# Kernel tuning notes

Measured on AMD Instinct MI355X. Metric: run time of the kernel, lower is better.

Reference implementation:

```python
import jax, jax.numpy as jnp
import numpy as np

# Multi-scale spatial shapes for a 704x256 input at strides 4/8/16/32
LEVEL_SHAPES = [(64, 176), (32, 88), (16, 44), (8, 22)]  # sum HW = 14960
NUM_CAMS, NUM_LEVELS, NUM_PTS, NUM_GROUPS = 6, 4, 13, 8
NUM_ANCHOR, EMBED_DIMS = 900, 256


def setup_inputs() -> dict:
    key = jax.random.key(0)
    ks = jax.random.split(key, 8)
    total_hw = sum(h * w for h, w in LEVEL_SHAPES)
    feat = jax.random.normal(ks[0], (1, NUM_CAMS, total_hw, EMBED_DIMS), jnp.float32)
    key_points = jax.random.uniform(ks[1], (1, NUM_ANCHOR, NUM_PTS, 3), jnp.float32)
    # near-identity projection so sampled locations spread over the image plane
    lidar2img = jnp.eye(4, dtype=jnp.float32)[None, None] + 0.05 * jax.random.normal(
        ks[2], (1, NUM_CAMS, 4, 4), jnp.float32)
    image_wh = jnp.ones((1, NUM_CAMS, 2), jnp.float32)
    instance_feature = jax.random.normal(ks[3], (1, NUM_ANCHOR, EMBED_DIMS), jnp.float32)
    anchor_embed = jax.random.normal(ks[4], (1, NUM_ANCHOR, EMBED_DIMS), jnp.float32)
    k_out = NUM_CAMS * NUM_LEVELS * NUM_PTS * NUM_GROUPS  # 2496
    weights_fc_w = jax.random.normal(ks[5], (k_out, EMBED_DIMS), jnp.float32) * 0.02
    weights_fc_b = jnp.zeros((k_out,), jnp.float32)
    out_proj_w = jax.random.normal(ks[6], (EMBED_DIMS, EMBED_DIMS), jnp.float32) * 0.02
    out_proj_b = jnp.zeros((EMBED_DIMS,), jnp.float32)
    return dict(feat=feat, key_points=key_points, lidar2img=lidar2img, image_wh=image_wh,
                instance_feature=instance_feature, anchor_embed=anchor_embed,
                weights_fc_w=weights_fc_w, weights_fc_b=weights_fc_b,
                out_proj_w=out_proj_w, out_proj_b=out_proj_b)


def _bilinear_sample(feat_flat, H, W, loc):
    # feat_flat: [bs, cams, H*W, C]; loc: [bs, cams, Q, 2] normalized to [0,1]
    x = loc[..., 0] * W - 0.5
    y = loc[..., 1] * H - 0.5
    x0 = jnp.floor(x); y0 = jnp.floor(y)
    wx1 = x - x0; wy1 = y - y0
    x0i = x0.astype(jnp.int32); y0i = y0.astype(jnp.int32)
    acc = jnp.zeros(loc.shape[:-1] + (feat_flat.shape[-1],), feat_flat.dtype)
    for dx, dy, w in ((0, 0, (1 - wx1) * (1 - wy1)), (1, 0, wx1 * (1 - wy1)),
                      (0, 1, (1 - wx1) * wy1), (1, 1, wx1 * wy1)):
        xi = x0i + dx; yi = y0i + dy
        valid = ((xi >= 0) & (xi < W) & (yi >= 0) & (yi < H)).astype(feat_flat.dtype)
        idx = jnp.clip(yi, 0, H - 1) * W + jnp.clip(xi, 0, W - 1)  # [bs, cams, Q]
        g = jnp.take_along_axis(feat_flat, idx[..., None], axis=2)  # [bs, cams, Q, C]
        acc = acc + g * (w * valid)[..., None]
    return acc


def reference(feat, key_points, lidar2img, image_wh, instance_feature, anchor_embed,
              weights_fc_w, weights_fc_b, out_proj_w, out_proj_b):
    bs, A, P = key_points.shape[:3]
    C, G, L, Ncam = EMBED_DIMS, NUM_GROUPS, NUM_LEVELS, NUM_CAMS
    # ---- _get_weights: fc + softmax over (cams*levels*pts) per group ----
    logits = jnp.einsum('bad,kd->bak', instance_feature + anchor_embed, weights_fc_w) + weights_fc_b
    w = jax.nn.softmax(logits.reshape(bs, A, -1, G), axis=-2)
    w = w.reshape(bs, A, Ncam, L, P, G).transpose(0, 1, 4, 2, 3, 5)  # [bs,A,P,cams,L,G]
    # ---- project_points ----
    pts_h = jnp.concatenate([key_points, jnp.ones_like(key_points[..., :1])], axis=-1)  # [bs,A,P,4]
    proj = jnp.einsum('bcij,bapj->bcapi', lidar2img, pts_h)  # [bs,cams,A,P,4]
    xy = proj[..., :2] / jnp.clip(proj[..., 2:3], 1e-5, None)
    pts2d = xy / image_wh[:, :, None, None, :]               # [bs,cams,A,P,2]
    loc = pts2d.reshape(bs, Ncam, A * P, 2)
    # ---- DAF: per-level bilinear sample + group-weighted reduction ----
    out_acc = jnp.zeros((bs, A, G, C // G), feat.dtype)
    start = 0
    for li, (H, W) in enumerate(LEVEL_SHAPES):
        fl = feat[:, :, start:start + H * W, :]
        s = _bilinear_sample(fl, H, W, loc)                   # [bs,cams,A*P,C]
        s = s.reshape(bs, Ncam, A, P, G, C // G)
        out_acc = out_acc + jnp.einsum('bapcg,bcapgd->bagd', w[..., li, :], s)
        start += H * W
    features = out_acc.reshape(bs, A, C)
    return features @ out_proj_w.T + out_proj_b  # output_proj
```

## Files before the change

### kernel.cpp

```cpp
#include <hip/hip_runtime.h>
#include <math.h>

#define EMBED   256
#define NCAM    6
#define NLVL    4
#define NPTS    13
#define NGRP    8
#define NANCH   900
#define NTERM   (NCAM*NLVL*NPTS)
#define KOUT    (NTERM*NGRP)
#define TOTHW   14960
#define SPLIT   4
#define TPS     (NTERM/SPLIT)

__global__ __launch_bounds__(256)
void gemm_bias_f32(const float* __restrict__ A0, const float* __restrict__ A1,
                   const float* __restrict__ B,  const float* __restrict__ bias,
                   float* __restrict__ Cout, int M, int N, int K)
{
    const int BK = 32;
    __shared__ alignas(16) float As[32][68];
    __shared__ alignas(16) float Bs[32][68];

    const int bm = blockIdx.y * 64;
    const int bn = blockIdx.x * 64;
    const int tid = threadIdx.x;
    const int tx = tid & 15;
    const int ty = tid >> 4;

    float acc[4][4] = {{0.f}};

    for (int k0 = 0; k0 < K; k0 += BK) {
        #pragma unroll
        for (int i = 0; i < 2; ++i) {
            int lin = (tid + i * 256) * 4;
            int r = lin >> 5;
            int cc = lin & 31;
            int gm = bm + r;
            float4 v = make_float4(0.f, 0.f, 0.f, 0.f);
            if (gm < M) {
                v = *reinterpret_cast<const float4*>(A0 + (size_t)gm * K + k0 + cc);
                if (A1) {
                    float4 v1 = *reinterpret_cast<const float4*>(A1 + (size_t)gm * K + k0 + cc);
                    v.x += v1.x; v.y += v1.y; v.z += v1.z; v.w += v1.w;
                }
            }
            As[cc + 0][r] = v.x; As[cc + 1][r] = v.y;
            As[cc + 2][r] = v.z; As[cc + 3][r] = v.w;

            int gn = bn + r;
            float4 w = make_float4(0.f, 0.f, 0.f, 0.f);
            if (gn < N) {
                w = *reinterpret_cast<const float4*>(B + (size_t)gn * K + k0 + cc);
            }
            Bs[cc + 0][r] = w.x; Bs[cc + 1][r] = w.y;
            Bs[cc + 2][r] = w.z; Bs[cc + 3][r] = w.w;
        }
        __syncthreads();

        #pragma unroll
        for (int k = 0; k < BK; ++k) {
            float4 a4 = *reinterpret_cast<const float4*>(&As[k][ty * 4]);
            float4 b4 = *reinterpret_cast<const float4*>(&Bs[k][tx * 4]);
            float a[4] = {a4.x, a4.y, a4.z, a4.w};
            float b[4] = {b4.x, b4.y, b4.z, b4.w};
            #pragma unroll
            for (int i = 0; i < 4; ++i)
                #pragma unroll
                for (int j = 0; j < 4; ++j)
                    acc[i][j] = fmaf(a[i], b[j], acc[i][j]);
        }
        __syncthreads();
    }

    #pragma unroll
    for (int i = 0; i < 4; ++i) {
        int m = bm + ty * 4 + i;
        if (m >= M) break;
        #pragma unroll
        for (int j = 0; j < 4; ++j) {
            int n = bn + tx * 4 + j;
            if (n < N) Cout[(size_t)m * N + n] = acc[i][j] + (bias ? bias[n] : 0.f);
        }
    }
}

__global__ __launch_bounds__(256)
void softmax_k(const float* __restrict__ logits,
               float* __restrict__ wsm,
               float* __restrict__ outacc)
{
    __shared__ alignas(16) float wl[KOUT];
    const int a   = blockIdx.x;
    const int tid = threadIdx.x;

    {
        const float4* src = reinterpret_cast<const float4*>(logits + (size_t)a * KOUT);
        float4* dst = reinterpret_cast<float4*>(wl);
        for (int i = tid; i < KOUT / 4; i += 256) dst[i] = src[i];
    }
    __syncthreads();

    int g = tid >> 5;
    int j = tid & 31;
    float mx = -1e30f;
    for (int m = j; m < NTERM; m += 32) mx = fmaxf(mx, wl[m * NGRP + g]);
    #pragma unroll
    for (int s = 16; s > 0; s >>= 1) mx = fmaxf(mx, __shfl_xor(mx, s, 32));
    float sum = 0.f;
    for (int m = j; m < NTERM; m += 32) {
        float e = __expf(wl[m * NGRP + g] - mx);
        wl[m * NGRP + g] = e;
        sum += e;
    }
    #pragma unroll
    for (int s = 16; s > 0; s >>= 1) sum += __shfl_xor(sum, s, 32);
    float inv = 1.f / sum;
    for (int m = j; m < NTERM; m += 32) wl[m * NGRP + g] *= inv;
    __syncthreads();

    {
        const float4* src = reinterpret_cast<const float4*>(wl);
        float4* dst = reinterpret_cast<float4*>(wsm + (size_t)a * KOUT);
        for (int i = tid; i < KOUT / 4; i += 256) dst[i] = src[i];
    }
    outacc[(size_t)a * EMBED + tid] = 0.f;
}

__global__ __launch_bounds__(256)
void sample_agg_split(const float* __restrict__ feat,
                      const float* __restrict__ key_points,
                      const float* __restrict__ lidar2img,
                      const float* __restrict__ image_wh,
                      const float* __restrict__ wsm,
                      float* __restrict__ outacc)
{
    __shared__ alignas(16) float wl[TPS * NGRP];
    __shared__ alignas(16) int   cidx[TPS][4];
    __shared__ alignas(16) float cwgt[TPS][4];
    __shared__ int tmap[TPS];
    __shared__ int ncomp;

    const int bid = blockIdx.x;
    const int a   = bid >> 2;
    const int sp  = bid & (SPLIT - 1);
    const int t0  = sp * TPS;
    const int tid = threadIdx.x;

    if (tid == 0) ncomp = 0;
    {
        const float4* src = reinterpret_cast<const float4*>(wsm + (size_t)a * KOUT + t0 * NGRP);
        float4* dst = reinterpret_cast<float4*>(wl);
        if (tid < TPS * NGRP / 4) dst[tid] = src[tid];
    }
    __syncthreads();

    if (tid < TPS) {
        int t = t0 + tid;
        int cam = t / (NLVL * NPTS);
        int rem = t - cam * (NLVL * NPTS);
        int lvl = rem / NPTS;
        int p   = rem - lvl * NPTS;

        const float* kp = key_points + ((size_t)a * NPTS + p) * 3;
        float px = kp[0], py = kp[1], pz = kp[2];
        const float* M4 = lidar2img + cam * 16;
        float X = M4[0] * px + M4[1] * py + M4[2]  * pz + M4[3];
        float Y = M4[4] * px + M4[5] * py + M4[6]  * pz + M4[7];
        float Z = M4[8] * px + M4[9] * py + M4[10] * pz + M4[11];
        float zc = fmaxf(Z, 1e-5f);
        float u = (X / zc) / image_wh[cam * 2 + 0];
        float v = (Y / zc) / image_wh[cam * 2 + 1];

        int H = 64 >> lvl, W = 176 >> lvl;
        int st = (lvl == 0) ? 0 : (lvl == 1) ? 11264 : (lvl == 2) ? 14080 : 14784;

        float x = u * (float)W - 0.5f;
        float y = v * (float)H - 0.5f;
        float x0f = floorf(x), y0f = floorf(y);
        float wx1 = x - x0f, wy1 = y - y0f;
        float wx0 = 1.f - wx1, wy0 = 1.f - wy1;
        int x0 = (int)x0f, y0 = (int)y0f;
        int x1 = x0 + 1,   y1 = y0 + 1;

        bool vx0 = (x0 >= 0) & (x0 < W), vx1 = (x1 >= 0) & (x1 < W);
        bool vy0 = (y0 >= 0) & (y0 < H), vy1 = (y1 >= 0) & (y1 < H);
        int cx0 = min(max(x0, 0), W - 1), cx1 = min(max(x1, 0), W - 1);
        int cy0 = min(max(y0, 0), H - 1), cy1 = min(max(y1, 0), H - 1);

        float w00 = wx0 * wy0 * ((vx0 & vy0) ? 1.f : 0.f);
        float w10 = wx1 * wy0 * ((vx1 & vy0) ? 1.f : 0.f);
        float w01 = wx0 * wy1 * ((vx0 & vy1) ? 1.f : 0.f);
        float w11 = wx1 * wy1 * ((vx1 & vy1) ? 1.f : 0.f);

        if ((w00 != 0.f) | (w10 != 0.f) | (w01 != 0.f) | (w11 != 0.f)) {
            int slot = atomicAdd(&ncomp, 1);
            int base = cam * TOTHW + st;
            cidx[slot][0] = (base + cy0 * W + cx0) * EMBED;
            cidx[slot][1] = (base + cy0 * W + cx1) * EMBED;
            cidx[slot][2] = (base + cy1 * W + cx0) * EMBED;
            cidx[slot][3] = (base + cy1 * W + cx1) * EMBED;
            cwgt[slot][0] = w00;
            cwgt[slot][1] = w10;
            cwgt[slot][2] = w01;
            cwgt[slot][3] = w11;
            tmap[slot] = tid;
        }
    }
    __syncthreads();

    const int c = tid;
    const int g = c >> 5;
    const int nt = ncomp;
    float acc = 0.f;
    const float* fbase = feat + c;

    #pragma unroll 4
    for (int s = 0; s < nt; ++s) {
        int4   I  = *reinterpret_cast<const int4*>(&cidx[s][0]);
        float4 Wt = *reinterpret_cast<const float4*>(&cwgt[s][0]);
        float  gw = wl[tmap[s] * NGRP + g];
        float v0 = fbase[I.x];
        float v1 = fbase[I.y];
        float v2 = fbase[I.z];
        float v3 = fbase[I.w];
        float sv = v0 * Wt.x + v1 * Wt.y + v2 * Wt.z + v3 * Wt.w;
        acc = fmaf(sv, gw, acc);
    }
    atomicAdd(&outacc[(size_t)a * EMBED + c], acc);
}

extern "C" void kernel_launch(void* const* d_in, const int* in_sizes, int n_in,
                              void* d_out, int out_size, void* d_ws, size_t ws_size,
                              hipStream_t stream)
{
    const float* feat   = (const float*)d_in[0];
    const float* kp     = (const float*)d_in[1];
    const float* l2i    = (const float*)d_in[2];
    const float* iwh    = (const float*)d_in[3];
    const float* inst   = (const float*)d_in[4];
    const float* anch   = (const float*)d_in[5];
    const float* wfc    = (const float*)d_in[6];
    const float* bfc    = (const float*)d_in[7];
    const float* wproj  = (const float*)d_in[8];
    const float* bproj  = (const float*)d_in[9];
    float* out = (float*)d_out;

    float* logits = (float*)d_ws;
    float* wsm    = logits + (size_t)NANCH * KOUT;
    float* outacc = wsm    + (size_t)NANCH * KOUT;

    {
        dim3 grid(KOUT / 64, (NANCH + 63) / 64);
        gemm_bias_f32<<<grid, 256, 0, stream>>>(inst, anch, wfc, bfc,
                                                logits, NANCH, KOUT, EMBED);
    }

    softmax_k<<<dim3(NANCH), 256, 0, stream>>>(logits, wsm, outacc);

    sample_agg_split<<<dim3(NANCH * SPLIT), 256, 0, stream>>>(feat, kp, l2i, iwh,
                                                              wsm, outacc);

    {
        dim3 grid(EMBED / 64, (NANCH + 63) / 64);
        gemm_bias_f32<<<grid, 256, 0, stream>>>(outacc, nullptr, wproj, bproj,
                                                out, NANCH, EMBED, EMBED);
    }
}
```

Before: 235.6 us.

## Fuse softmax into sampling kernel and replace atomics with split-partial sum in projection GEMM

Removes the separate softmax kernel. Each sampling block now recomputes the full per-anchor softmax from the logits in shared memory, using a padded stride to reduce bank conflicts. The atomicAdd accumulation and the zeroing of the accumulator are replaced by writing four partial outputs per anchor. The output-projection GEMM sums these four partials while loading its A tile. This saves one launch and the round trip of the softmax weights through global memory, but each of the four split blocks now redoes the full softmax (4x the softmax work) and reads all logits.

```diff
diff --git a/kernel.cpp b/kernel.cpp
--- a/kernel.cpp
+++ b/kernel.cpp
@@ -12,6 +12,7 @@
 #define TOTHW   14960
 #define SPLIT   4
 #define TPS     (NTERM/SPLIT)
+#define WSTR    9
 
 __global__ __launch_bounds__(256)
 void gemm_bias_f32(const float* __restrict__ A0, const float* __restrict__ A1,
@@ -86,56 +87,91 @@
 }
 
 __global__ __launch_bounds__(256)
-void softmax_k(const float* __restrict__ logits,
-               float* __restrict__ wsm,
-               float* __restrict__ outacc)
+void gemm_bias_sum4_f32(const float* __restrict__ Ap,
+                        const float* __restrict__ B, const float* __restrict__ bias,
+                        float* __restrict__ Cout, int M, int N, int K)
 {
-    __shared__ alignas(16) float wl[KOUT];
-    const int a   = blockIdx.x;
+    const int BK = 32;
+    __shared__ alignas(16) float As[32][68];
+    __shared__ alignas(16) float Bs[32][68];
+
+    const int bm = blockIdx.y * 64;
+    const int bn = blockIdx.x * 64;
     const int tid = threadIdx.x;
-
-    {
-        const float4* src = reinterpret_cast<const float4*>(logits + (size_t)a * KOUT);
-        float4* dst = reinterpret_cast<float4*>(wl);
-        for (int i = tid; i < KOUT / 4; i += 256) dst[i] = src[i];
-    }
-    __syncthreads();
-
-    int g = tid >> 5;
-    int j = tid & 31;
-    float mx = -1e30f;
-    for (int m = j; m < NTERM; m += 32) mx = fmaxf(mx, wl[m * NGRP + g]);
+    const int tx = tid & 15;
+    const int ty = tid >> 4;
+    const size_t pstride = (size_t)M * K;
+
+    float acc[4][4] = {{0.f}};
+
+    for (int k0 = 0; k0 < K; k0 += BK) {
+        #pragma unroll
+        for (int i = 0; i < 2; ++i) {
+            int lin = (tid + i * 256) * 4;
+            int r = lin >> 5;
+            int cc = lin & 31;
+            int gm = bm + r;
+            float4 v = make_float4(0.f, 0.f, 0.f, 0.f);
+            if (gm < M) {
+                const float* p = Ap + (size_t)gm * K + k0 + cc;
+                float4 v0 = *reinterpret_cast<const float4*>(p);
+                float4 v1 = *reinterpret_cast<const float4*>(p + pstride);
+                float4 v2 = *reinterpret_cast<const float4*>(p + 2 * pstride);
+                float4 v3 = *reinterpret_cast<const float4*>(p + 3 * pstride);
+                v.x = v0.x + v1.x + v2.x + v3.x;
+                v.y = v0.y + v1.y + v2.y + v3.y;
+                v.z = v0.z + v1.z + v2.z + v3.z;
+                v.w = v0.w + v1.w + v2.w + v3.w;
+            }
+            As[cc + 0][r] = v.x; As[cc + 1][r] = v.y;
+            As[cc + 2][r] = v.z; As[cc + 3][r] = v.w;
+
+            int gn = bn + r;
+            float4 w = make_float4(0.f, 0.f, 0.f, 0.f);
+            if (gn < N) {
+                w = *reinterpret_cast<const float4*>(B + (size_t)gn * K + k0 + cc);
+            }
+            Bs[cc + 0][r] = w.x; Bs[cc + 1][r] = w.y;
+            Bs[cc + 2][r] = w.z; Bs[cc + 3][r] = w.w;
+        }
+        __syncthreads();
+
+        #pragma unroll
+        for (int k = 0; k < BK; ++k) {
+            float4 a4 = *reinterpret_cast<const float4*>(&As[k][ty * 4]);
+            float4 b4 = *reinterpret_cast<const float4*>(&Bs[k][tx * 4]);
+            float a[4] = {a4.x, a4.y, a4.z, a4.w};
+            float b[4] = {b4.x, b4.y, b4.z, b4.w};
+            #pragma unroll
+            for (int i = 0; i < 4; ++i)
+                #pragma unroll
+                for (int j = 0; j < 4; ++j)
+                    acc[i][j] = fmaf(a[i], b[j], acc[i][j]);
+        }
+        __syncthreads();
+    }
+
     #pragma unroll
-    for (int s = 16; s > 0; s >>= 1) mx = fmaxf(mx, __shfl_xor(mx, s, 32));
-    float sum = 0.f;
-    for (int m = j; m < NTERM; m += 32) {
-        float e = __expf(wl[m * NGRP + g] - mx);
-        wl[m * NGRP + g] = e;
-        sum += e;
-    }
-    #pragma unroll
-    for (int s = 16; s > 0; s >>= 1) sum += __shfl_xor(sum, s, 32);
-    float inv = 1.f / sum;
-    for (int m = j; m < NTERM; m += 32) wl[m * NGRP + g] *= inv;
-    __syncthreads();
-
-    {
-        const float4* src = reinterpret_cast<const float4*>(wl);
-        float4* dst = reinterpret_cast<float4*>(wsm + (size_t)a * KOUT);
-        for (int i = tid; i < KOUT / 4; i += 256) dst[i] = src[i];
-    }
-    outacc[(size_t)a * EMBED + tid] = 0.f;
+    for (int i = 0; i < 4; ++i) {
+        int m = bm + ty * 4 + i;
+        if (m >= M) break;
+        #pragma unroll
+        for (int j = 0; j < 4; ++j) {
+            int n = bn + tx * 4 + j;
+            if (n < N) Cout[(size_t)m * N + n] = acc[i][j] + (bias ? bias[n] : 0.f);
+        }
+    }
 }
 
 __global__ __launch_bounds__(256)
-void sample_agg_split(const float* __restrict__ feat,
+void sample_agg_fused(const float* __restrict__ feat,
                       const float* __restrict__ key_points,
                       const float* __restrict__ lidar2img,
                       const float* __restrict__ image_wh,
-                      const float* __restrict__ wsm,
-                      float* __restrict__ outacc)
+                      const float* __restrict__ logits,
+                      float* __restrict__ outpart)
 {
-    __shared__ alignas(16) float wl[TPS * NGRP];
+    __shared__ float wl[NTERM * WSTR];
     __shared__ alignas(16) int   cidx[TPS][4];
     __shared__ alignas(16) float cwgt[TPS][4];
     __shared__ int tmap[TPS];
@@ -148,12 +184,40 @@
     const int tid = threadIdx.x;
 
     if (tid == 0) ncomp = 0;
+
     {
-        const float4* src = reinterpret_cast<const float4*>(wsm + (size_t)a * KOUT + t0 * NGRP);
-        float4* dst = reinterpret_cast<float4*>(wl);
-        if (tid < TPS * NGRP / 4) dst[tid] = src[tid];
+        const float4* src = reinterpret_cast<const float4*>(logits + (size_t)a * KOUT);
+        for (int i = tid; i < KOUT / 4; i += 256) {
+            float4 v = src[i];
+            int e = i * 4;
+            float vv[4] = {v.x, v.y, v.z, v.w};
+            #pragma unroll
+            for (int q = 0; q < 4; ++q) {
+                int m = (e + q) >> 3, g = (e + q) & 7;
+                wl[m * WSTR + g] = vv[q];
+            }
+        }
     }
     __syncthreads();
+
+    {
+        int g = tid >> 5;
+        int j = tid & 31;
+        float mx = -1e30f;
+        for (int m = j; m < NTERM; m += 32) mx = fmaxf(mx, wl[m * WSTR + g]);
+        #pragma unroll
+        for (int s = 16; s > 0; s >>= 1) mx = fmaxf(mx, __shfl_xor(mx, s, 32));
+        float sum = 0.f;
+        for (int m = j; m < NTERM; m += 32) {
+            float e = __expf(wl[m * WSTR + g] - mx);
+            wl[m * WSTR + g] = e;
+            sum += e;
+        }
+        #pragma unroll
+        for (int s = 16; s > 0; s >>= 1) sum += __shfl_xor(sum, s, 32);
+        float inv = 1.f / sum;
+        for (int m = j; m < NTERM; m += 32) wl[m * WSTR + g] *= inv;
+    }
 
     if (tid < TPS) {
         int t = t0 + tid;
@@ -219,7 +283,7 @@
     for (int s = 0; s < nt; ++s) {
         int4   I  = *reinterpret_cast<const int4*>(&cidx[s][0]);
         float4 Wt = *reinterpret_cast<const float4*>(&cwgt[s][0]);
-        float  gw = wl[tmap[s] * NGRP + g];
+        float  gw = wl[(t0 + tmap[s]) * WSTR + g];
         float v0 = fbase[I.x];
         float v1 = fbase[I.y];
         float v2 = fbase[I.z];
@@ -227,7 +291,7 @@
         float sv = v0 * Wt.x + v1 * Wt.y + v2 * Wt.z + v3 * Wt.w;
         acc = fmaf(sv, gw, acc);
     }
-    atomicAdd(&outacc[(size_t)a * EMBED + c], acc);
+    outpart[((size_t)sp * NANCH + a) * EMBED + c] = acc;
 }
 
 extern "C" void kernel_launch(void* const* d_in, const int* in_sizes, int n_in,
@@ -246,9 +310,8 @@
     const float* bproj  = (const float*)d_in[9];
     float* out = (float*)d_out;
 
-    float* logits = (float*)d_ws;
-    float* wsm    = logits + (size_t)NANCH * KOUT;
-    float* outacc = wsm    + (size_t)NANCH * KOUT;
+    float* logits  = (float*)d_ws;
+    float* outpart = logits + (size_t)NANCH * KOUT;
 
     {
         dim3 grid(KOUT / 64, (NANCH + 63) / 64);
@@ -256,14 +319,12 @@
                                                 logits, NANCH, KOUT, EMBED);
     }
 
-    softmax_k<<<dim3(NANCH), 256, 0, stream>>>(logits, wsm, outacc);
-
-    sample_agg_split<<<dim3(NANCH * SPLIT), 256, 0, stream>>>(feat, kp, l2i, iwh,
-                                                              wsm, outacc);
+    sample_agg_fused<<<dim3(NANCH * SPLIT), 256, 0, stream>>>(feat, kp, l2i, iwh,
+                                                              logits, outpart);
 
     {
         dim3 grid(EMBED / 64, (NANCH + 63) / 64);
-        gemm_bias_f32<<<grid, 256, 0, stream>>>(outacc, nullptr, wproj, bproj,
-                                                out, NANCH, EMBED, EMBED);
+        gemm_bias_sum4_f32<<<grid, 256, 0, stream>>>(outpart, wproj, bproj,
+                                                     out, NANCH, EMBED, EMBED);
     }
 }
```

New measurement: 234.1 us. Within noise of the previous version (-0.7%).
